# Performance work log

Measured on AMD Instinct MI355X. Metric: run time of the kernel, lower is better.

The kernel has to match this reference:

```python
import jax, jax.numpy as jnp
import numpy as np
from jax import lax

D = 4            # shift radius
NSHIFT = 2 * D + 1  # 9 shifts per axis -> 81 total


def setup_inputs() -> dict:
    key = jax.random.key(0)
    k1, k2, k3, k4, k5, k6 = jax.random.split(key, 6)
    B, C, H, W = 4, 256, 64, 128
    R = 16  # reduction ratio
    feat1 = jax.random.normal(k1, (B, C, H, W), dtype=jnp.float32)
    feat2 = jax.random.normal(k2, (B, C, H, W), dtype=jnp.float32)
    # ca_conv1: Conv2d(C, C//R, 1) -> weight [C//R, C], bias [C//R]
    w1 = jax.random.normal(k3, (C // R, C), dtype=jnp.float32) * (1.0 / np.sqrt(C))
    b1 = jax.random.normal(k4, (C // R,), dtype=jnp.float32) * 0.01
    # ca_conv2: Conv2d(C//R, C, 1) -> weight [C, C//R], bias [C]
    w2 = jax.random.normal(k5, (C, C // R), dtype=jnp.float32) * (1.0 / np.sqrt(C // R))
    b2 = jax.random.normal(k6, (C,), dtype=jnp.float32) * 0.01
    return {"feat1": feat1, "feat2": feat2, "w1": w1, "b1": b1, "w2": w2, "b2": b2}


def reference(feat1, feat2, w1, b1, w2, b2):
    B, C, H, W = feat1.shape
    # zero-pad feat2 spatially by D on each side (matches F.pad constant 0)
    feat2p = jnp.pad(feat2, ((0, 0), (0, 0), (D, D), (D, D)))

    def one_shift(carry, idx):
        i = idx // NSHIFT
        j = idx % NSHIFT
        f2 = lax.dynamic_slice(feat2p, (0, 0, i, j), (B, C, H, W))
        sim = feat1 * f2                              # [B,C,H,W]
        pooled = jnp.mean(sim, axis=(2, 3))           # global avg pool -> [B,C]
        a = pooled @ w1.T + b1                        # [B,C//R] (1x1 conv == matmul)
        a = a @ w2.T + b2                             # [B,C]
        a = jax.nn.sigmoid(a)
        out = jnp.mean(a[:, :, None, None] * sim, axis=1)  # channel mean -> [B,H,W]
        return carry, out

    _, cv = lax.scan(one_shift, None, jnp.arange(NSHIFT * NSHIFT))  # [81,B,H,W]
    return jnp.transpose(cv, (1, 0, 2, 3))  # [B,81,H,W]
```

## Files before the change

### kernel.cpp

```cpp
#include <hip/hip_runtime.h>
#include <math.h>


#define HH 64
#define WW 128
#define CC 256
#define BB 4

__global__ __launch_bounds__(576) void corr_pool_kernel(
    const float* __restrict__ f1, const float* __restrict__ f2,
    float* __restrict__ pooled) {
  const int t  = threadIdx.x;
  const int bc = blockIdx.x;
  const float* f1p = f1 + (size_t)bc * (HH * WW);
  const float* f2p = f2 + (size_t)bc * (HH * WW);

  __shared__ float4 f2s4[72 * 35];

  const float4 z4 = make_float4(0.f, 0.f, 0.f, 0.f);
  for (int u = t; u < 72 * 35; u += 576) {
    const int rl = u / 35, k = u - rl * 35;
    const int gr = rl - 4;
    float4 v = z4;
    if ((unsigned)gr < 64u && k >= 1 && k <= 32)
      v = *(const float4*)(f2p + (gr << 7) + ((k - 1) << 2));
    f2s4[u] = v;
  }
  __syncthreads();

  const int h  = t / 9;
  const int di = t - h * 9;
  const float4* f2row = &f2s4[(h + di) * 35];
  const float* f1row  = f1p + (h << 7);

  float s9[9];
#pragma unroll
  for (int j = 0; j < 9; ++j) s9[j] = 0.f;

  alignas(16) float f1c[16], f2wc[24];
#pragma unroll
  for (int m = 0; m < 4; ++m)
    *(float4*)&f1c[4 * m] = *(const float4*)(f1row + (m << 2));
#pragma unroll
  for (int m = 0; m < 6; ++m) *(float4*)&f2wc[4 * m] = f2row[m];

  for (int seg = 0; seg < 8; ++seg) {
    const int nxt = (seg < 7) ? seg + 1 : 7;
    alignas(16) float f1n[16], f2wn[24];
#pragma unroll
    for (int m = 0; m < 4; ++m)
      *(float4*)&f1n[4 * m] =
          *(const float4*)(f1row + (nxt << 4) + (m << 2));
#pragma unroll
    for (int m = 0; m < 6; ++m) *(float4*)&f2wn[4 * m] = f2row[(nxt << 2) + m];

#pragma unroll
    for (int k = 0; k < 16; ++k) {
      const float a = f1c[k];
#pragma unroll
      for (int j = 0; j < 9; ++j) s9[j] += a * f2wc[k + j];
    }
#pragma unroll
    for (int m = 0; m < 16; ++m) f1c[m] = f1n[m];
#pragma unroll
    for (int m = 0; m < 24; ++m) f2wc[m] = f2wn[m];
  }

  __syncthreads();
  float* red  = (float*)f2s4;
  float* red2 = red + 64 * 81;
#pragma unroll
  for (int j = 0; j < 9; ++j) red[h * 81 + di * 9 + j] = s9[j];
  __syncthreads();

  if (t < 567) {
    const int col = t % 81, g = t / 81;
    const int r0 = g * 9, r1 = (g == 6) ? 64 : r0 + 9;
    float acc = 0.f;
#pragma unroll 3
    for (int rr = r0; rr < r1; ++rr) acc += red[rr * 81 + col];
    red2[g * 81 + col] = acc;
  }
  __syncthreads();

  if (t < 81) {
    float acc = 0.f;
#pragma unroll
    for (int g = 0; g < 7; ++g) acc += red2[g * 81 + t];
    const int b = bc >> 8, c = bc & 255;
    pooled[(size_t)(b * 81 + t) * 256 + c] = acc;
  }
}

__global__ __launch_bounds__(256) void mlp_kernel(
    const float* __restrict__ pooled, const float* __restrict__ w1,
    const float* __restrict__ b1, const float* __restrict__ w2,
    const float* __restrict__ b2, float* __restrict__ At) {
  const int bs = blockIdx.x;
  const int t  = threadIdx.x;
  const int b  = bs / 81;
  const int s  = bs - b * 81;
  __shared__ float p[256];
  __shared__ float hid[16];

  p[t] = pooled[(size_t)bs * 256 + t] * (1.0f / 8192.0f);
  __syncthreads();

  const int g = t >> 4, ln = t & 15;
  float acc = 0.f;
#pragma unroll
  for (int m = 0; m < 16; ++m) {
    const int c = (m << 4) + ln;
    acc += w1[(g << 8) + c] * p[c];
  }
  acc += __shfl_xor(acc, 1);
  acc += __shfl_xor(acc, 2);
  acc += __shfl_xor(acc, 4);
  acc += __shfl_xor(acc, 8);
  if (ln == 0) hid[g] = acc + b1[g];
  __syncthreads();

  float acc2 = b2[t];
#pragma unroll
  for (int k = 0; k < 16; ++k) acc2 += w2[(t << 4) + k] * hid[k];
  const float sv = 1.0f / (1.0f + __expf(-acc2));
  At[((size_t)(b * 256 + t)) * 81 + s] = sv;
}

__global__ __launch_bounds__(64, 4) void out_kernel(
    const float* __restrict__ f1, const float* __restrict__ f2,
    const float* __restrict__ At, float* __restrict__ out,
    float* __restrict__ part) {
  const int bid  = blockIdx.x;
  const int x    = bid & 7;
  const int q    = bid >> 3;
  const int i    = q % 9;
  const int tq   = q / 9;
  const int tile = tq * 8 + x;
  const int half = tile & 1;
  const int rt   = (tile >> 1) & 31;
  const int b    = tile >> 6;
  const int h0   = rt << 1;

  const int t    = threadIdx.x;
  const int r    = t >> 5;
  const int cidx = t & 31;
  const int w0   = cidx << 2;
  const int h    = h0 + r;
  const int hr   = h + i - 4;
  const bool rowok = ((unsigned)hr < 64u);

  float acc[9][4];
#pragma unroll
  for (int j = 0; j < 9; ++j)
#pragma unroll
    for (int k = 0; k < 4; ++k) acc[j][k] = 0.f;

  if (rowok) {
    const int c0 = half << 7;
    const float* pa1 = f1 + (size_t)b * (CC * 8192) + (size_t)c0 * 8192 +
                       (h << 7) + w0;
    const float* pa2 = f2 + (size_t)b * (CC * 8192) + (size_t)c0 * 8192 +
                       (hr << 7);
    const float* pb1 = pa1 + (size_t)64 * 8192;
    const float* pb2 = pa2 + (size_t)64 * 8192;
    const float* Aa  = At + (size_t)b * (CC * 81) + (size_t)c0 * 81 + i * 9;

    const bool vA  = (cidx > 0);
    const bool vC  = (cidx < 31);
    const int ofsA = vA ? (w0 - 4) : 0;
    const int ofsC = vC ? (w0 + 4) : 120;

    for (int c = 0; c < 64; ++c) {
      const float4 xa = *(const float4*)(pa1);
      const float4 aA = *(const float4*)(pa2 + ofsA);
      const float4 aB = *(const float4*)(pa2 + w0);
      const float4 aC = *(const float4*)(pa2 + ofsC);
      const float4 xb = *(const float4*)(pb1);
      const float4 bA = *(const float4*)(pb2 + ofsA);
      const float4 bB = *(const float4*)(pb2 + w0);
      const float4 bC = *(const float4*)(pb2 + ofsC);

      const float* ca = Aa + (size_t)c * 81;
      const float* cb = ca + (size_t)64 * 81;

      const int adv = (c < 63) ? 8192 : 0;
      pa1 += adv; pa2 += adv; pb1 += adv; pb2 += adv;

      alignas(16) float f2ra[12];
      f2ra[0] = vA ? aA.x : 0.f;
      f2ra[1] = vA ? aA.y : 0.f;
      f2ra[2] = vA ? aA.z : 0.f;
      f2ra[3] = vA ? aA.w : 0.f;
      f2ra[4] = aB.x; f2ra[5] = aB.y; f2ra[6] = aB.z; f2ra[7] = aB.w;
      f2ra[8]  = vC ? aC.x : 0.f;
      f2ra[9]  = vC ? aC.y : 0.f;
      f2ra[10] = vC ? aC.z : 0.f;
      f2ra[11] = vC ? aC.w : 0.f;
      alignas(16) const float xxa[4] = {xa.x, xa.y, xa.z, xa.w};

#pragma unroll
      for (int j = 0; j < 9; ++j) {
        const float wj = ca[j];
#pragma unroll
        for (int k = 0; k < 4; ++k) acc[j][k] += wj * (xxa[k] * f2ra[k + j]);
      }

      alignas(16) float f2rb[12];
      f2rb[0] = vA ? bA.x : 0.f;
      f2rb[1] = vA ? bA.y : 0.f;
      f2rb[2] = vA ? bA.z : 0.f;
      f2rb[3] = vA ? bA.w : 0.f;
      f2rb[4] = bB.x; f2rb[5] = bB.y; f2rb[6] = bB.z; f2rb[7] = bB.w;
      f2rb[8]  = vC ? bC.x : 0.f;
      f2rb[9]  = vC ? bC.y : 0.f;
      f2rb[10] = vC ? bC.z : 0.f;
      f2rb[11] = vC ? bC.w : 0.f;
      alignas(16) const float xxb[4] = {xb.x, xb.y, xb.z, xb.w};

#pragma unroll
      for (int j = 0; j < 9; ++j) {
        const float wj = cb[j];
#pragma unroll
        for (int k = 0; k < 4; ++k) acc[j][k] += wj * (xxb[k] * f2rb[k + j]);
      }
    }
  }

  float* dst = half ? part : out;
  const float inv = 1.0f / 256.0f;
#pragma unroll
  for (int j = 0; j < 9; ++j) {
    float4 o;
    o.x = acc[j][0] * inv;
    o.y = acc[j][1] * inv;
    o.z = acc[j][2] * inv;
    o.w = acc[j][3] * inv;
    *(float4*)(dst + (((size_t)(b * 81 + i * 9 + j) * 64 + h) << 7) + w0) = o;
  }
}

__global__ __launch_bounds__(256) void combine_kernel(
    float* __restrict__ out, const float* __restrict__ part) {
  const size_t idx = (size_t)blockIdx.x * 256 + threadIdx.x;
  float4* o4       = (float4*)out;
  const float4* p4 = (const float4*)part;
  const float4 a = o4[idx], p = p4[idx];
  float4 rv;
  rv.x = a.x + p.x; rv.y = a.y + p.y; rv.z = a.z + p.z; rv.w = a.w + p.w;
  o4[idx] = rv;
}

extern "C" void kernel_launch(void* const* d_in, const int* in_sizes, int n_in,
                              void* d_out, int out_size, void* d_ws, size_t ws_size,
                              hipStream_t stream) {
  const float* feat1 = (const float*)d_in[0];
  const float* feat2 = (const float*)d_in[1];
  const float* w1    = (const float*)d_in[2];
  const float* b1    = (const float*)d_in[3];
  const float* w2    = (const float*)d_in[4];
  const float* b2    = (const float*)d_in[5];
  float* out = (float*)d_out;

  float* pooled = (float*)d_ws;
  float* At     = pooled + 82944;
  float* cpart  = At + 82944;

  corr_pool_kernel<<<1024, 576, 0, stream>>>(feat1, feat2, pooled);
  mlp_kernel<<<4 * 81, 256, 0, stream>>>(pooled, w1, b1, w2, b2, At);
  out_kernel<<<2304, 64, 0, stream>>>(feat1, feat2, At, out, cpart);
  combine_kernel<<<2592, 256, 0, stream>>>(out, cpart);
}
```

Measured before the change: 192.5 us.

## Split channel reduction across four waves with shared-memory combine, drop combine kernel

The output kernel now uses 256-thread blocks in which four wavefronts each handle 64 channels of the same tile. Partial sums are reduced through shared memory instead of being written to a global partial buffer and added by a separate combine kernel. This removes one kernel launch and the extra global round trip of the full output-sized partial array. In exchange it adds a block barrier and shared-memory traffic, and the register budget changes with the new launch bounds.

```diff
diff --git a/kernel.cpp b/kernel.cpp
--- a/kernel.cpp
+++ b/kernel.cpp
@@ -127,43 +127,43 @@
   At[((size_t)(b * 256 + t)) * 81 + s] = sv;
 }
 
-__global__ __launch_bounds__(64, 4) void out_kernel(
+__global__ __launch_bounds__(256, 5) void out_kernel(
     const float* __restrict__ f1, const float* __restrict__ f2,
-    const float* __restrict__ At, float* __restrict__ out,
-    float* __restrict__ part) {
+    const float* __restrict__ At, float* __restrict__ out) {
   const int bid  = blockIdx.x;
   const int x    = bid & 7;
   const int q    = bid >> 3;
   const int i    = q % 9;
   const int tq   = q / 9;
   const int tile = tq * 8 + x;
-  const int half = tile & 1;
-  const int rt   = (tile >> 1) & 31;
-  const int b    = tile >> 6;
+  const int rt   = tile & 31;
+  const int b    = tile >> 5;
   const int h0   = rt << 1;
 
   const int t    = threadIdx.x;
-  const int r    = t >> 5;
-  const int cidx = t & 31;
+  const int wv   = t >> 6;
+  const int lane = t & 63;
+  const int r    = lane >> 5;
+  const int cidx = lane & 31;
   const int w0   = cidx << 2;
   const int h    = h0 + r;
   const int hr   = h + i - 4;
   const bool rowok = ((unsigned)hr < 64u);
 
-  float acc[9][4];
+  alignas(16) float acc[9][4];
 #pragma unroll
   for (int j = 0; j < 9; ++j)
 #pragma unroll
     for (int k = 0; k < 4; ++k) acc[j][k] = 0.f;
 
   if (rowok) {
-    const int c0 = half << 7;
+    const int c0 = wv << 6;
     const float* pa1 = f1 + (size_t)b * (CC * 8192) + (size_t)c0 * 8192 +
                        (h << 7) + w0;
     const float* pa2 = f2 + (size_t)b * (CC * 8192) + (size_t)c0 * 8192 +
                        (hr << 7);
-    const float* pb1 = pa1 + (size_t)64 * 8192;
-    const float* pb2 = pa2 + (size_t)64 * 8192;
+    const float* pb1 = pa1 + (size_t)32 * 8192;
+    const float* pb2 = pa2 + (size_t)32 * 8192;
     const float* Aa  = At + (size_t)b * (CC * 81) + (size_t)c0 * 81 + i * 9;
 
     const bool vA  = (cidx > 0);
@@ -171,7 +171,7 @@
     const int ofsA = vA ? (w0 - 4) : 0;
     const int ofsC = vC ? (w0 + 4) : 120;
 
-    for (int c = 0; c < 64; ++c) {
+    for (int c = 0; c < 32; ++c) {
       const float4 xa = *(const float4*)(pa1);
       const float4 aA = *(const float4*)(pa2 + ofsA);
       const float4 aB = *(const float4*)(pa2 + w0);
@@ -182,9 +182,9 @@
       const float4 bC = *(const float4*)(pb2 + ofsC);
 
       const float* ca = Aa + (size_t)c * 81;
-      const float* cb = ca + (size_t)64 * 81;
-
-      const int adv = (c < 63) ? 8192 : 0;
+      const float* cb = ca + (size_t)32 * 81;
+
+      const int adv = (c < 31) ? 8192 : 0;
       pa1 += adv; pa2 += adv; pb1 += adv; pb2 += adv;
 
       alignas(16) float f2ra[12];
@@ -227,28 +227,37 @@
     }
   }
 
-  float* dst = half ? part : out;
-  const float inv = 1.0f / 256.0f;
-#pragma unroll
-  for (int j = 0; j < 9; ++j) {
-    float4 o;
-    o.x = acc[j][0] * inv;
-    o.y = acc[j][1] * inv;
-    o.z = acc[j][2] * inv;
-    o.w = acc[j][3] * inv;
-    *(float4*)(dst + (((size_t)(b * 81 + i * 9 + j) * 64 + h) << 7) + w0) = o;
-  }
-}
-
-__global__ __launch_bounds__(256) void combine_kernel(
-    float* __restrict__ out, const float* __restrict__ part) {
-  const size_t idx = (size_t)blockIdx.x * 256 + threadIdx.x;
-  float4* o4       = (float4*)out;
-  const float4* p4 = (const float4*)part;
-  const float4 a = o4[idx], p = p4[idx];
-  float4 rv;
-  rv.x = a.x + p.x; rv.y = a.y + p.y; rv.z = a.z + p.z; rv.w = a.w + p.w;
-  o4[idx] = rv;
+  __shared__ float4 red4[27][64];
+  if (wv > 0) {
+#pragma unroll
+    for (int j = 0; j < 9; ++j)
+      red4[(wv - 1) * 9 + j][lane] = *(const float4*)&acc[j][0];
+  }
+  __syncthreads();
+
+  if (wv == 0) {
+#pragma unroll
+    for (int v = 0; v < 3; ++v)
+#pragma unroll
+      for (int j = 0; j < 9; ++j) {
+        const float4 p = red4[v * 9 + j][lane];
+        acc[j][0] += p.x;
+        acc[j][1] += p.y;
+        acc[j][2] += p.z;
+        acc[j][3] += p.w;
+      }
+
+    const float inv = 1.0f / 256.0f;
+#pragma unroll
+    for (int j = 0; j < 9; ++j) {
+      float4 o;
+      o.x = acc[j][0] * inv;
+      o.y = acc[j][1] * inv;
+      o.z = acc[j][2] * inv;
+      o.w = acc[j][3] * inv;
+      *(float4*)(out + (((size_t)(b * 81 + i * 9 + j) * 64 + h) << 7) + w0) = o;
+    }
+  }
 }
 
 extern "C" void kernel_launch(void* const* d_in, const int* in_sizes, int n_in,
@@ -264,10 +273,8 @@
 
   float* pooled = (float*)d_ws;
   float* At     = pooled + 82944;
-  float* cpart  = At + 82944;
 
   corr_pool_kernel<<<1024, 576, 0, stream>>>(feat1, feat2, pooled);
   mlp_kernel<<<4 * 81, 256, 0, stream>>>(pooled, w1, b1, w2, b2, At);
-  out_kernel<<<2304, 64, 0, stream>>>(feat1, feat2, At, out, cpart);
-  combine_kernel<<<2592, 256, 0, stream>>>(out, cpart);
-}
+  out_kernel<<<1152, 256, 0, stream>>>(feat1, feat2, At, out);
+}
```

New measurement: 198.7 us. 3.2% more time.

## Double-buffer out_kernel channel loads into LDS with async global_load_lds

Applied to the files above, without the earlier changes.

The out_kernel inner channel loop now prefetches the next channel's feat1 and feat2 rows straight into a double-buffered LDS tile with `__builtin_amdgcn_global_load_lds`, waiting with explicit `s_waitcnt vmcnt`. Horizontal neighbours for the shifted window are read from adjacent lanes' LDS entries instead of three overlapping global float4 loads per row. The aim is to overlap global memory latency with the FMA work and to cut redundant global and L1 traffic. In exchange it relies on hand-written vmcnt accounting that shares the counter with the compiler-managed loads of the At weights. It also issues one redundant prefetch on the final iteration.

```diff
diff --git a/kernel.cpp b/kernel.cpp
--- a/kernel.cpp
+++ b/kernel.cpp
@@ -125,6 +125,12 @@
   for (int k = 0; k < 16; ++k) acc2 += w2[(t << 4) + k] * hid[k];
   const float sv = 1.0f / (1.0f + __expf(-acc2));
   At[((size_t)(b * 256 + t)) * 81 + s] = sv;
+}
+
+__device__ __forceinline__ void async16(const float* g, void* lds) {
+  __builtin_amdgcn_global_load_lds(
+      (const __attribute__((address_space(1))) void*)g,
+      (__attribute__((address_space(3))) void*)lds, 16, 0, 0);
 }
 
 __global__ __launch_bounds__(64, 4) void out_kernel(
@@ -150,6 +156,8 @@
   const int hr   = h + i - 4;
   const bool rowok = ((unsigned)hr < 64u);
 
+  __shared__ float4 sb[2][4][64];
+
   float acc[9][4];
 #pragma unroll
   for (int j = 0; j < 9; ++j)
@@ -168,24 +176,39 @@
 
     const bool vA  = (cidx > 0);
     const bool vC  = (cidx < 31);
-    const int ofsA = vA ? (w0 - 4) : 0;
-    const int ofsC = vC ? (w0 + 4) : 120;
+    const int lane = t;
+    const int lm1  = vA ? lane - 1 : lane;
+    const int lp1  = vC ? lane + 1 : lane;
+
+    async16(pa1,      &sb[0][0][0]);
+    async16(pb1,      &sb[0][1][0]);
+    async16(pa2 + w0, &sb[0][2][0]);
+    async16(pb2 + w0, &sb[0][3][0]);
 
     for (int c = 0; c < 64; ++c) {
-      const float4 xa = *(const float4*)(pa1);
-      const float4 aA = *(const float4*)(pa2 + ofsA);
-      const float4 aB = *(const float4*)(pa2 + w0);
-      const float4 aC = *(const float4*)(pa2 + ofsC);
-      const float4 xb = *(const float4*)(pb1);
-      const float4 bA = *(const float4*)(pb2 + ofsA);
-      const float4 bB = *(const float4*)(pb2 + w0);
-      const float4 bC = *(const float4*)(pb2 + ofsC);
+      const int cur = c & 1;
+      const int nxt = cur ^ 1;
+
+      const int adv = (c < 63) ? 8192 : 0;
+      pa1 += adv; pa2 += adv; pb1 += adv; pb2 += adv;
+      async16(pa1,      &sb[nxt][0][0]);
+      async16(pb1,      &sb[nxt][1][0]);
+      async16(pa2 + w0, &sb[nxt][2][0]);
+      async16(pb2 + w0, &sb[nxt][3][0]);
+
+      asm volatile("s_waitcnt vmcnt(4)" ::: "memory");
+
+      const float4 xa = sb[cur][0][lane];
+      const float4 xb = sb[cur][1][lane];
+      const float4 aA = sb[cur][2][lm1];
+      const float4 aB = sb[cur][2][lane];
+      const float4 aC = sb[cur][2][lp1];
+      const float4 bA = sb[cur][3][lm1];
+      const float4 bB = sb[cur][3][lane];
+      const float4 bC = sb[cur][3][lp1];
 
       const float* ca = Aa + (size_t)c * 81;
       const float* cb = ca + (size_t)64 * 81;
-
-      const int adv = (c < 63) ? 8192 : 0;
-      pa1 += adv; pa2 += adv; pb1 += adv; pb2 += adv;
 
       alignas(16) float f2ra[12];
       f2ra[0] = vA ? aA.x : 0.f;
@@ -225,6 +248,8 @@
         for (int k = 0; k < 4; ++k) acc[j][k] += wj * (xxb[k] * f2rb[k + j]);
       }
     }
+
+    asm volatile("s_waitcnt vmcnt(0)" ::: "memory");
   }
 
   float* dst = half ? part : out;
```

Result: no change. 192.8 us (+0.2%).
